# Kernel tuning notes

Hardware: AMD Instinct MI355X
Metric: run time of the kernel (lower is better)

The kernel has to match this reference:

```python
import jax, jax.numpy as jnp
import numpy as np

N_NODES = 100000
N_EDGES = 1600000
N_GRAPHS = 512
EPS = 1e-12


def _glorot(key, shape):
    lim = float(np.sqrt(6.0 / (shape[0] + shape[1])))
    return jax.random.uniform(key, shape, jnp.float32, -lim, lim)


def setup_inputs() -> dict:
    key = jax.random.key(0)
    ks = jax.random.split(key, 16)
    x = jax.random.normal(ks[0], (N_NODES, 5), jnp.float32)
    edge_index = jax.random.randint(ks[1], (2, N_EDGES), 0, N_NODES)
    batch = jnp.sort(jax.random.randint(ks[2], (N_NODES,), 0, N_GRAPHS))
    return {
        "x": x,
        "edge_index": edge_index,
        "batch": batch,
        "num_graphs": N_GRAPHS,
        # pre: Linear(5, 32)
        "pre_w": _glorot(ks[3], (5, 32)), "pre_b": jnp.zeros((32,), jnp.float32),
        # conv1: SAGEConv(32, 64): lin_l (agg, bias), lin_r (root, no bias)
        "c1_wl": _glorot(ks[4], (32, 64)), "c1_bl": jnp.zeros((64,), jnp.float32),
        "c1_wr": _glorot(ks[5], (32, 64)),
        # conv2: SAGEConv(64, 64)
        "c2_wl": _glorot(ks[6], (64, 64)), "c2_bl": jnp.zeros((64,), jnp.float32),
        "c2_wr": _glorot(ks[7], (64, 64)),
        # post / out linears
        "p1_w": _glorot(ks[8], (64, 64)), "p1_b": jnp.zeros((64,), jnp.float32),
        "p2_w": _glorot(ks[9], (64, 16)), "p2_b": jnp.zeros((16,), jnp.float32),
        "o_w": _glorot(ks[10], (16, 1)), "o_b": jnp.zeros((1,), jnp.float32),
    }


def _sage_conv(x, src, dst, w_l, b_l, w_r, n_nodes):
    # mean-aggregate neighbor messages src -> dst
    msg = x[src]                                              # [E, d]
    agg = jax.ops.segment_sum(msg, dst, num_segments=n_nodes)  # [N, d]
    cnt = jax.ops.segment_sum(jnp.ones((src.shape[0], 1), x.dtype), dst,
                              num_segments=n_nodes)            # [N, 1]
    agg = jnp.where(cnt > 0, agg / jnp.maximum(cnt, 1.0), 0.0)
    out = agg @ w_l + b_l + x @ w_r
    # normalize=True -> L2 normalize per node
    nrm = jnp.linalg.norm(out, axis=-1, keepdims=True)
    return out / jnp.maximum(nrm, EPS)


def reference(x, edge_index, batch, num_graphs,
              pre_w, pre_b, c1_wl, c1_bl, c1_wr, c2_wl, c2_bl, c2_wr,
              p1_w, p1_b, p2_w, p2_b, o_w, o_b):
    n_nodes = x.shape[0]
    src, dst = edge_index[0], edge_index[1]
    h = jax.nn.relu(x @ pre_w + pre_b)
    h = jax.nn.relu(_sage_conv(h, src, dst, c1_wl, c1_bl, c1_wr, n_nodes))
    h = jax.nn.relu(_sage_conv(h, src, dst, c2_wl, c2_bl, c2_wr, n_nodes))
    # global mean pool over batch index
    s = jax.ops.segment_sum(h, batch, num_segments=num_graphs)          # [G, d]
    c = jax.ops.segment_sum(jnp.ones((n_nodes, 1), h.dtype), batch,
                            num_segments=num_graphs)                    # [G, 1]
    g = s / jnp.maximum(c, 1.0)
    g = jax.nn.relu(g @ p1_w + p1_b)
    g = jax.nn.relu(g @ p2_w + p2_b)
    out = g @ o_w + o_b
    return out.squeeze(-1)
```

## Files before the change

kernel.cpp:

```cpp
#include <hip/hip_runtime.h>

#define EPSN 1e-12f
#define TILE 2048
#define BSH 8
#define BNODES 256
#define SBMAX 512
#define BCAP 4608

using frag_ab = __attribute__((ext_vector_type(8))) short;
using frag_cd = __attribute__((ext_vector_type(4))) float;

__device__ inline unsigned short f2bf(float x) {
    union { float f; unsigned u; } v; v.f = x;
    unsigned r = v.u + 0x7fffu + ((v.u >> 16) & 1u);
    return (unsigned short)(r >> 16);
}
__device__ inline float bf2f(unsigned short b) {
    union { unsigned u; float f; } v; v.u = ((unsigned)b) << 16; return v.f;
}
__device__ inline void upadd2(uint2 u, float* a) {
    a[0] += bf2f((unsigned short)u.x); a[1] += bf2f((unsigned short)(u.x >> 16));
    a[2] += bf2f((unsigned short)u.y); a[3] += bf2f((unsigned short)(u.y >> 16));
}

__global__ __launch_bounds__(256) void prep_all(
    const float* __restrict__ x, const float* __restrict__ pw,
    const float* __restrict__ pb, unsigned short* __restrict__ h0, int n,
    const float* __restrict__ w1l, const float* __restrict__ w1r,
    unsigned short* __restrict__ wpk1,
    const float* __restrict__ w2l, const float* __restrict__ w2r,
    unsigned short* __restrict__ wpk2,
    float* __restrict__ sg, int gtot,
    const int* __restrict__ dst, int* __restrict__ thistT, int e,
    int nsb, int nt) {
    __shared__ int lh[SBMAX];
    int tid = threadIdx.x;
    if (blockIdx.x < nt) {
        int b = blockIdx.x;
        for (int i = tid; i < nsb; i += 256) lh[i] = 0;
        __syncthreads();
        int base = b * TILE, lim = min(base + TILE, e);
        for (int i = base + tid; i < lim; i += 256) atomicAdd(&lh[dst[i] >> BSH], 1);
        __syncthreads();
        for (int i = tid; i < nsb; i += 256) thistT[(size_t)b * nsb + i] = lh[i];
        return;
    }
    int idx = (blockIdx.x - nt) * 256 + tid;
    int npre = n * 32;
    if (idx < npre) {
        int node = idx >> 5, j = idx & 31;
        float v = pb[j];
#pragma unroll
        for (int k = 0; k < 5; ++k) v += x[node * 5 + k] * pw[k * 32 + j];
        h0[idx] = f2bf(fmaxf(v, 0.f));
        return;
    }
    int o = idx - npre;
    if (o < 64 * 64) {
        int j = o / 64, k = o % 64;
        float v = (k < 32) ? w1l[k * 64 + j] : w1r[(k - 32) * 64 + j];
        wpk1[o] = f2bf(v);
        return;
    }
    o -= 64 * 64;
    if (o < 64 * 128) {
        int j = o / 128, k = o % 128;
        float v = (k < 64) ? w2l[k * 64 + j] : w2r[(k - 64) * 64 + j];
        wpk2[o] = f2bf(v);
        return;
    }
    o -= 64 * 128;
    if (o < gtot) sg[o] = 0.f;
}

__global__ __launch_bounds__(256) void tscan_k(const int* __restrict__ thistT,
                                               int* __restrict__ toffsT,
                                               int* __restrict__ btot,
                                               int nsb, int nt) {
    __shared__ int wsum[8];
    int b = blockIdx.x;
    int tid = threadIdx.x;
    int lane = tid & 63, w = tid >> 6;
    int run = 0;
    for (int base = 0; base < nt; base += 256) {
        int i = base + tid;
        int x = (i < nt) ? thistT[(size_t)i * nsb + b] : 0;
        int inc = x;
#pragma unroll
        for (int o = 1; o < 64; o <<= 1) {
            int t = __shfl_up(inc, o);
            if (lane >= o) inc += t;
        }
        if (lane == 63) wsum[w] = inc;
        __syncthreads();
        if (tid == 0) {
            int s = 0;
#pragma unroll
            for (int k = 0; k < 4; ++k) { int t = wsum[k]; wsum[k] = s; s += t; }
            wsum[4] = s;
        }
        __syncthreads();
        if (i < nt) toffsT[(size_t)b * nt + i] = inc - x + wsum[w] + run;
        run += wsum[4];
        __syncthreads();
    }
    if (tid == 0) btot[b] = run;
}

__global__ __launch_bounds__(256) void scat1_k(const int* __restrict__ src,
                                               const int* __restrict__ dst,
                                               const int* __restrict__ toffsT,
                                               int* __restrict__ staged, int e,
                                               int nsb, int nt) {
    __shared__ int cur[SBMAX];
    int tid = threadIdx.x;
    for (int i = tid; i < nsb; i += 256)
        cur[i] = i * BCAP + toffsT[(size_t)i * nt + blockIdx.x];
    __syncthreads();
    int base = blockIdx.x * TILE;
    int lim = min(base + TILE, e);
    for (int i = base + tid; i < lim; i += 256) {
        int d = dst[i];
        int p = atomicAdd(&cur[d >> BSH], 1);
        staged[p] = (src[i] << BSH) | (d & (BNODES - 1));
    }
}

__global__ __launch_bounds__(256) void scat2_k(const int* __restrict__ btot,
                                               const int* __restrict__ staged,
                                               int* __restrict__ csr,
                                               int* __restrict__ rofs,
                                               int* __restrict__ deg,
                                               int n, int nsb) {
    __shared__ int h[BNODES];
    __shared__ int cur[BNODES];
    __shared__ int wsum[8];
    int b = blockIdx.x;
    int tid = threadIdx.x;
    int lane = tid & 63, w = tid >> 6;
    int nlo = b << BSH;
    int nn = n - nlo; if (nn > BNODES) nn = BNODES;
    int lo = b * BCAP, hi = lo + btot[b];
    h[tid] = 0;
    __syncthreads();
    for (int i = lo + tid; i < hi; i += 256) atomicAdd(&h[staged[i] & (BNODES - 1)], 1);
    __syncthreads();
    int x = h[tid];
    int inc = x;
#pragma unroll
    for (int o = 1; o < 64; o <<= 1) {
        int t = __shfl_up(inc, o);
        if (lane >= o) inc += t;
    }
    if (lane == 63) wsum[w] = inc;
    __syncthreads();
    if (tid == 0) {
        int s = 0;
#pragma unroll
        for (int k = 0; k < 4; ++k) { int t = wsum[k]; wsum[k] = s; s += t; }
    }
    __syncthreads();
    int excl = inc - x + wsum[w];
    cur[tid] = excl;
    if (tid < nn) {
        rofs[nlo + tid] = lo + excl;
        deg[nlo + tid] = x;
    }
    __syncthreads();
    for (int i = lo + tid; i < hi; i += 256) {
        int v = staged[i];
        int p = atomicAdd(&cur[v & (BNODES - 1)], 1);
        csr[lo + p] = v >> BSH;
    }
}

template <int KIN, bool POOL>
__global__ __launch_bounds__(256) void conv_mfma(
    const int* __restrict__ rofs, const int* __restrict__ deg,
    const int* __restrict__ csr,
    const unsigned short* __restrict__ hin, const unsigned short* __restrict__ wpk,
    const float* __restrict__ bl, const int* __restrict__ batch,
    float* __restrict__ sg, unsigned short* __restrict__ hout, int n) {
    constexpr int KT = 2 * KIN;
    constexpr int ST = KT + 8;
    constexpr int KS = KT / 32;
    constexpr int LPE = KIN / 4;
    constexpr int EPW = 64 / LPE;
    constexpr int RB = 4;
    __shared__ unsigned short __attribute__((aligned(16))) Ab[16 * ST];
    __shared__ float __attribute__((aligned(16))) Nb[4][16];
    __shared__ int ro[16];
    __shared__ int dg[16];
    __shared__ int sb[16];

    int tid = threadIdx.x;
    int w = tid >> 6;
    int lane = tid & 63;
    int quad = lane >> 4;
    int l16 = lane & 15;
    int base = blockIdx.x * 16;
    int ncol = w * 16 + l16;

    if (tid < 16) {
        int nd = base + tid;
        bool v = nd < n;
        ro[tid] = v ? rofs[nd] : 0;
        dg[tid] = v ? deg[nd] : 0;
        if (POOL) sb[tid] = v ? batch[nd] : -1;
    }

    frag_ab bfrag[KS];
#pragma unroll
    for (int s = 0; s < KS; ++s)
        bfrag[s] = *(const frag_ab*)&wpk[(((ncol * KS) + s) * 4 + quad) * 8];
    float bias = bl[ncol];
    __syncthreads();

    int grp = lane / LPE;
    int p = lane % LPE;
    for (int i = 0; i < 4; ++i) {
        int li = w * 4 + i;
        int node = base + li;
        if (node >= n) break;
        int beg = ro[li];
        int cnt = dg[li];
        uint2 selfv = make_uint2(0u, 0u);
        if (grp == 1)
            selfv = *(const uint2*)&hin[(size_t)node * KIN + p * 4];
        float a[4] = {0.f, 0.f, 0.f, 0.f};
        for (int e0 = 0; e0 < cnt; e0 += RB * EPW) {
            int idx[RB];
            uint2 u[RB];
#pragma unroll
            for (int r = 0; r < RB; ++r) {
                int ee = e0 + r * EPW + grp;
                int cl = (ee < cnt) ? ee : (cnt - 1);
                idx[r] = csr[beg + cl];
            }
#pragma unroll
            for (int r = 0; r < RB; ++r)
                u[r] = *(const uint2*)&hin[(size_t)idx[r] * KIN + p * 4];
#pragma unroll
            for (int r = 0; r < RB; ++r)
                if (e0 + r * EPW + grp < cnt) upadd2(u[r], a);
        }
#pragma unroll
        for (int o = LPE; o < 64; o <<= 1) {
#pragma unroll
            for (int q = 0; q < 4; ++q) a[q] += __shfl_xor(a[q], o);
        }
        float inv = (cnt > 0) ? 1.0f / (float)cnt : 0.0f;
        if (grp == 0) {
            uint2 o2;
            o2.x = (unsigned)f2bf(a[0] * inv) | ((unsigned)f2bf(a[1] * inv) << 16);
            o2.y = (unsigned)f2bf(a[2] * inv) | ((unsigned)f2bf(a[3] * inv) << 16);
            *(uint2*)&Ab[li * ST + p * 4] = o2;
        } else if (grp == 1) {
            *(uint2*)&Ab[li * ST + KIN + p * 4] = selfv;
        }
    }
    __syncthreads();

    frag_cd acc = (frag_cd){0.f, 0.f, 0.f, 0.f};
#pragma unroll
    for (int s = 0; s < KS; ++s) {
        frag_ab af = *(frag_ab*)&Ab[l16 * ST + s * 32 + quad * 8];
        acc = __builtin_amdgcn_mfma_f32_16x16x32_bf16(af, bfrag[s], acc, 0, 0, 0);
    }

    float vv[4], q[4];
#pragma unroll
    for (int i = 0; i < 4; ++i) {
        float v = acc[i] + bias;
        vv[i] = v;
        q[i] = v * v;
    }
#pragma unroll
    for (int o = 1; o < 16; o <<= 1) {
#pragma unroll
        for (int i = 0; i < 4; ++i) q[i] += __shfl_xor(q[i], o);
    }
    if (l16 == 0)
        *(float4*)&Nb[w][quad * 4] = make_float4(q[0], q[1], q[2], q[3]);
    __syncthreads();

    float s0 = 0.f, s1 = 0.f, s2 = 0.f, s3 = 0.f;
#pragma unroll
    for (int ww = 0; ww < 4; ++ww) {
        float4 xq = *(const float4*)&Nb[ww][quad * 4];
        s0 += xq.x; s1 += xq.y; s2 += xq.z; s3 += xq.w;
    }
    float ss[4] = {s0, s1, s2, s3};
    float pv[4];
#pragma unroll
    for (int i = 0; i < 4; ++i) {
        float nv = fmaxf(sqrtf(ss[i]), EPSN);
        pv[i] = fmaxf(vv[i] / nv, 0.f);
    }

    if (!POOL) {
#pragma unroll
        for (int i = 0; i < 4; ++i) {
            int node = base + quad * 4 + i;
            if (node < n)
                hout[(size_t)node * 64 + ncol] = f2bf(pv[i]);
        }
    } else {
        int g0 = sb[0];
        int g1 = sb[min(15, n - 1 - base)];
        for (int g = g0; g <= g1; ++g) {
            float s = 0.f;
#pragma unroll
            for (int i = 0; i < 4; ++i)
                if (sb[quad * 4 + i] == g) s += pv[i];
            s += __shfl_xor(s, 16);
            s += __shfl_xor(s, 32);
            if (quad == 0) atomicAdd(&sg[(size_t)g * 64 + ncol], s);
        }
    }
}

__global__ __launch_bounds__(64) void mlp_k(
    const float* __restrict__ sg, const int* __restrict__ batch, int n,
    const float* __restrict__ p1w, const float* __restrict__ p1b,
    const float* __restrict__ p2w, const float* __restrict__ p2b,
    const float* __restrict__ ow, const float* __restrict__ ob,
    float* __restrict__ out) {
    __shared__ float gmean[64];
    __shared__ float a1[64];
    __shared__ float a2[16];
    int g = blockIdx.x;
    int j = threadIdx.x;
    int lo = 0, hi = n;
    while (lo < hi) { int m = (lo + hi) >> 1; if (batch[m] < g) lo = m + 1; else hi = m; }
    int start = lo;
    hi = n;
    while (lo < hi) { int m = (lo + hi) >> 1; if (batch[m] < g + 1) lo = m + 1; else hi = m; }
    float c = (float)(lo - start);
    gmean[j] = sg[(size_t)g * 64 + j] / fmaxf(c, 1.0f);
    __syncthreads();
    float v = p1b[j];
#pragma unroll 8
    for (int k = 0; k < 64; ++k) v = fmaf(gmean[k], p1w[k * 64 + j], v);
    a1[j] = fmaxf(v, 0.f);
    __syncthreads();
    if (j < 16) {
        float v2 = p2b[j];
#pragma unroll 8
        for (int k = 0; k < 64; ++k) v2 = fmaf(a1[k], p2w[k * 16 + j], v2);
        a2[j] = fmaxf(v2, 0.f);
    }
    __syncthreads();
    if (j == 0) {
        float v3 = ob[0];
#pragma unroll
        for (int k = 0; k < 16; ++k) v3 = fmaf(a2[k], ow[k], v3);
        out[g] = v3;
    }
}

extern "C" void kernel_launch(void* const* d_in, const int* in_sizes, int n_in,
                              void* d_out, int out_size, void* d_ws, size_t ws_size,
                              hipStream_t stream) {
    const float* x     = (const float*)d_in[0];
    const int*   ei    = (const int*)d_in[1];
    const int*   batch = (const int*)d_in[2];
    const float* pre_w = (const float*)d_in[4];
    const float* pre_b = (const float*)d_in[5];
    const float* c1_wl = (const float*)d_in[6];
    const float* c1_bl = (const float*)d_in[7];
    const float* c1_wr = (const float*)d_in[8];
    const float* c2_wl = (const float*)d_in[9];
    const float* c2_bl = (const float*)d_in[10];
    const float* c2_wr = (const float*)d_in[11];
    const float* p1w   = (const float*)d_in[12];
    const float* p1b   = (const float*)d_in[13];
    const float* p2w   = (const float*)d_in[14];
    const float* p2b   = (const float*)d_in[15];
    const float* ow    = (const float*)d_in[16];
    const float* ob    = (const float*)d_in[17];

    const int N = in_sizes[0] / 5;
    const int E = in_sizes[1] / 2;
    const int G = out_size;
    const int NT = (E + TILE - 1) / TILE;
    const int NSB = (N + BNODES - 1) / BNODES;
    const int* src = ei;
    const int* dst = ei + E;

    unsigned short* h0u = (unsigned short*)d_ws;
    unsigned short* h1u = h0u + (size_t)N * 32;
    unsigned short* wpk1 = h1u + (size_t)N * 64;
    unsigned short* wpk2 = wpk1 + 64 * 64;
    float* sg    = (float*)(wpk2 + 64 * 128);
    int* rofs    = (int*)(sg + (size_t)G * 64);
    int* deg     = rofs + N;
    int* btot    = deg + N;
    int* thistT  = btot + NSB;
    int* toffsT  = thistT + (size_t)NT * NSB;
    int* staged  = toffsT + (size_t)NSB * NT;
    int* csr     = staged + (size_t)NSB * BCAP;

    int prep_tot = N * 32 + 64 * 64 + 64 * 128 + G * 64;
    int prep_blocks = (prep_tot + 255) / 256;
    prep_all<<<NT + prep_blocks, 256, 0, stream>>>(
        x, pre_w, pre_b, h0u, N, c1_wl, c1_wr, wpk1, c2_wl, c2_wr, wpk2,
        sg, G * 64, dst, thistT, E, NSB, NT);

    tscan_k<<<NSB, 256, 0, stream>>>(thistT, toffsT, btot, NSB, NT);
    scat1_k<<<NT, 256, 0, stream>>>(src, dst, toffsT, staged, E, NSB, NT);
    scat2_k<<<NSB, 256, 0, stream>>>(btot, staged, csr, rofs, deg, N, NSB);

    conv_mfma<32, false><<<(N + 15) / 16, 256, 0, stream>>>(
        rofs, deg, csr, h0u, wpk1, c1_bl, batch, sg, h1u, N);
    conv_mfma<64, true><<<(N + 15) / 16, 256, 0, stream>>>(
        rofs, deg, csr, h1u, wpk2, c2_bl, batch, sg, nullptr, N);

    mlp_k<<<G, 64, 0, stream>>>(sg, batch, N, p1w, p1b, p2w, p2b, ow, ob,
                                (float*)d_out);
}
```

Measured before the change: 251.3 us.

## Stage block CSR slice in LDS and interleave gathers across four nodes per warp

```diff
diff --git a/kernel.cpp b/kernel.cpp
--- a/kernel.cpp
+++ b/kernel.cpp
@@ -6,9 +6,12 @@
 #define BNODES 256
 #define SBMAX 512
 #define BCAP 4608
+#define CSRCAP 512
 
 using frag_ab = __attribute__((ext_vector_type(8))) short;
 using frag_cd = __attribute__((ext_vector_type(4))) float;
+
+template <bool B> struct BoolC { static constexpr bool value = B; };
 
 __device__ inline unsigned short f2bf(float x) {
     union { float f; unsigned u; } v; v.f = x;
@@ -186,12 +189,14 @@
     constexpr int KS = KT / 32;
     constexpr int LPE = KIN / 4;
     constexpr int EPW = 64 / LPE;
-    constexpr int RB = 4;
+    constexpr int RB = 16 / EPW;
+    constexpr bool G4 = (LPE == 16);
     __shared__ unsigned short __attribute__((aligned(16))) Ab[16 * ST];
     __shared__ float __attribute__((aligned(16))) Nb[4][16];
     __shared__ int ro[16];
     __shared__ int dg[16];
     __shared__ int sb[16];
+    __shared__ int csrL[CSRCAP];
 
     int tid = threadIdx.x;
     int w = tid >> 6;
@@ -216,47 +221,104 @@
     float bias = bl[ncol];
     __syncthreads();
 
+    int ro0 = ro[0];
+    int lastv = min(15, n - 1 - base);
+    int span = ro[lastv] + dg[lastv] - ro0;
+    int spanL = min(span, CSRCAP);
+    for (int i = tid; i < spanL; i += 256) csrL[i] = csr[ro0 + i];
+
     int grp = lane / LPE;
     int p = lane % LPE;
+    int beg[4], cnt[4];
+#pragma unroll
     for (int i = 0; i < 4; ++i) {
         int li = w * 4 + i;
+        beg[i] = ro[li] - ro0;
+        cnt[i] = dg[li];
+    }
+
+    int sn = G4 ? grp : (grp & 3);
+    bool doSelf = G4 || (grp >= 4);
+    bool doAgg = G4 || (grp < 4);
+    int snode = base + w * 4 + sn;
+    uint2 selfv = make_uint2(0u, 0u);
+    if (doSelf && snode < n)
+        selfv = *(const uint2*)&hin[(size_t)snode * KIN + p * 4];
+    __syncthreads();
+
+    float A[4][4] = {{0.f, 0.f, 0.f, 0.f}, {0.f, 0.f, 0.f, 0.f},
+                     {0.f, 0.f, 0.f, 0.f}, {0.f, 0.f, 0.f, 0.f}};
+
+    auto run_sweeps = [&](auto uselc) {
+        constexpr bool USEL = decltype(uselc)::value;
+        for (int s = 0;; ++s) {
+            int e0 = s * 16;
+            uint2 u[4][RB];
+            bool act[4];
+#pragma unroll
+            for (int i = 0; i < 4; ++i) {
+                act[i] = e0 < cnt[i];
+                if (act[i]) {
+#pragma unroll
+                    for (int r = 0; r < RB; ++r) {
+                        int ee = e0 + r * EPW + grp;
+                        int cl = (ee < cnt[i]) ? ee : (cnt[i] - 1);
+                        int off = beg[i] + cl;
+                        int idx;
+                        if (USEL || off < CSRCAP) idx = csrL[off];
+                        else idx = csr[ro0 + off];
+                        u[i][r] = *(const uint2*)&hin[(size_t)idx * KIN + p * 4];
+                    }
+                }
+            }
+#pragma unroll
+            for (int i = 0; i < 4; ++i) {
+                if (act[i]) {
+#pragma unroll
+                    for (int r = 0; r < RB; ++r)
+                        if (e0 + r * EPW + grp < cnt[i]) upadd2(u[i][r], A[i]);
+                }
+            }
+            bool more = false;
+#pragma unroll
+            for (int i = 0; i < 4; ++i) more |= (e0 + 16) < cnt[i];
+            if (!more) break;
+        }
+    };
+    if (span <= CSRCAP) run_sweeps(BoolC<true>{});
+    else run_sweeps(BoolC<false>{});
+
+#pragma unroll
+    for (int i = 0; i < 4; ++i) {
+#pragma unroll
+        for (int o = LPE; o < 64; o <<= 1) {
+#pragma unroll
+            for (int q = 0; q < 4; ++q) A[i][q] += __shfl_xor(A[i][q], o);
+        }
+    }
+
+    float av0 = A[0][0], av1 = A[0][1], av2 = A[0][2], av3 = A[0][3];
+    int cs = cnt[0];
+#pragma unroll
+    for (int i = 1; i < 4; ++i) {
+        bool m = (sn == i);
+        av0 = m ? A[i][0] : av0; av1 = m ? A[i][1] : av1;
+        av2 = m ? A[i][2] : av2; av3 = m ? A[i][3] : av3;
+        cs = m ? cnt[i] : cs;
+    }
+    {
+        int li = w * 4 + sn;
         int node = base + li;
-        if (node >= n) break;
-        int beg = ro[li];
-        int cnt = dg[li];
-        uint2 selfv = make_uint2(0u, 0u);
-        if (grp == 1)
-            selfv = *(const uint2*)&hin[(size_t)node * KIN + p * 4];
-        float a[4] = {0.f, 0.f, 0.f, 0.f};
-        for (int e0 = 0; e0 < cnt; e0 += RB * EPW) {
-            int idx[RB];
-            uint2 u[RB];
-#pragma unroll
-            for (int r = 0; r < RB; ++r) {
-                int ee = e0 + r * EPW + grp;
-                int cl = (ee < cnt) ? ee : (cnt - 1);
-                idx[r] = csr[beg + cl];
+        if (node < n) {
+            if (doAgg) {
+                float inv = (cs > 0) ? 1.0f / (float)cs : 0.0f;
+                uint2 o2;
+                o2.x = (unsigned)f2bf(av0 * inv) | ((unsigned)f2bf(av1 * inv) << 16);
+                o2.y = (unsigned)f2bf(av2 * inv) | ((unsigned)f2bf(av3 * inv) << 16);
+                *(uint2*)&Ab[li * ST + p * 4] = o2;
             }
-#pragma unroll
-            for (int r = 0; r < RB; ++r)
-                u[r] = *(const uint2*)&hin[(size_t)idx[r] * KIN + p * 4];
-#pragma unroll
-            for (int r = 0; r < RB; ++r)
-                if (e0 + r * EPW + grp < cnt) upadd2(u[r], a);
-        }
-#pragma unroll
-        for (int o = LPE; o < 64; o <<= 1) {
-#pragma unroll
-            for (int q = 0; q < 4; ++q) a[q] += __shfl_xor(a[q], o);
-        }
-        float inv = (cnt > 0) ? 1.0f / (float)cnt : 0.0f;
-        if (grp == 0) {
-            uint2 o2;
-            o2.x = (unsigned)f2bf(a[0] * inv) | ((unsigned)f2bf(a[1] * inv) << 16);
-            o2.y = (unsigned)f2bf(a[2] * inv) | ((unsigned)f2bf(a[3] * inv) << 16);
-            *(uint2*)&Ab[li * ST + p * 4] = o2;
-        } else if (grp == 1) {
-            *(uint2*)&Ab[li * ST + KIN + p * 4] = selfv;
+            if (doSelf)
+                *(uint2*)&Ab[li * ST + KIN + p * 4] = selfv;
         }
     }
     __syncthreads();
```

Result: no change. 250.1 us (-0.5%).
